# Optimization experiments

Hardware: AMD Instinct MI355X
Metric: run time of the kernel (lower is better)

Reference implementation:

```python
import jax, jax.numpy as jnp
import numpy as np

N_S = 50000   # support points
N_Q = 50000   # query points
H = 32        # neighbors per query
K = 15        # kernel points
C_IN = 64
C_OUT = 64
G = 8         # group norm groups
RADIUS = 1.0
SIGMA = 0.6
EPS = 1e-5
NEG_SLOPE = 0.1


def setup_inputs() -> dict:
    key = jax.random.key(0)
    ks = jax.random.split(key, 8)
    s_feats = jax.random.normal(ks[0], (N_S, C_IN), jnp.float32)
    q_points = jax.random.uniform(ks[1], (N_Q, 3), jnp.float32)
    s_points = jax.random.uniform(ks[2], (N_S, 3), jnp.float32)
    # index N_S is the shadow (padding) neighbor
    neighbor_indices = jax.random.randint(ks[3], (N_Q, H), 0, N_S + 1)
    # kernel point dispositions: fixed points inside a ball of RADIUS
    d = jax.random.normal(ks[4], (K, 3), jnp.float32)
    d = d / jnp.linalg.norm(d, axis=1, keepdims=True)
    r = jax.random.uniform(ks[5], (K, 1), jnp.float32) ** (1.0 / 3.0)
    kernel_points = d * r * RADIUS                      # (K,3)
    weights = jax.random.normal(ks[6], (K, C_IN, C_OUT), jnp.float32) * (1.0 / np.sqrt(K * C_IN))
    bias = jax.random.normal(ks[7], (C_OUT,), jnp.float32) * 0.01
    gamma = jnp.ones((C_OUT,), jnp.float32)
    beta = jnp.zeros((C_OUT,), jnp.float32)
    return dict(s_feats=s_feats, q_points=q_points, s_points=s_points,
                neighbor_indices=neighbor_indices, kernel_points=kernel_points,
                weights=weights, bias=bias, gamma=gamma, beta=beta)


def kpconv(s_feats, q_points, s_points, neighbor_indices, kernel_points, weights, bias):
    # pad support set with shadow point (1e10) and zero features
    pad_pts = jnp.concatenate([s_points, jnp.full((1, 3), 1e10, s_points.dtype)], axis=0)
    pad_feats = jnp.concatenate([s_feats, jnp.zeros((1, s_feats.shape[1]), s_feats.dtype)], axis=0)
    nbr_pts = pad_pts[neighbor_indices] - q_points[:, None, :]              # (M,H,3)
    diff = nbr_pts[:, :, None, :] - kernel_points[None, None, :, :]         # (M,H,K,3)
    sq_d = jnp.sum(diff * diff, axis=-1)                                    # (M,H,K)
    # linear correlation influence, clamped at 0
    w = jnp.maximum(1.0 - jnp.sqrt(sq_d) / SIGMA, 0.0)                      # (M,H,K)
    nbr_feats = pad_feats[neighbor_indices]                                 # (M,H,Cin)
    weighted = jnp.einsum('mhk,mhc->mkc', w, nbr_feats)                     # (M,K,Cin)
    out = jnp.einsum('mkc,kcd->md', weighted, weights)                      # (M,Cout)
    # normalize by number of valid neighbors (feature-sum > 0 test, as in KPConv)
    nbr_num = jnp.sum(jnp.sum(nbr_feats, axis=-1) > 0, axis=-1)             # (M,)
    nbr_num = jnp.maximum(nbr_num, 1).astype(out.dtype)
    return out / nbr_num[:, None] + bias


def group_norm(x, gamma, beta):
    # matches GroupNorm wrapper: (M,C) -> (1,C,M) -> nn.GroupNorm -> (M,C)
    M, C = x.shape
    xg = x.T.reshape(G, C // G, M)                                          # (G,Cg,M)
    mean = xg.mean(axis=(1, 2), keepdims=True)
    var = xg.var(axis=(1, 2), keepdims=True)
    xn = ((xg - mean) / jnp.sqrt(var + EPS)).reshape(C, M).T                # (M,C)
    return xn * gamma + beta


def reference(s_feats, q_points, s_points, neighbor_indices, kernel_points, weights, bias, gamma, beta):
    x = kpconv(s_feats, q_points, s_points, neighbor_indices, kernel_points, weights, bias)
    x = group_norm(x, gamma, beta)
    x = jnp.where(x >= 0, x, NEG_SLOPE * x)                                 # LeakyReLU(0.1)
    return x[:, None, :]                                                    # unsqueeze(1): (M,1,Cout)
```

## Files before the change

kernel.cpp:

```cpp
#include <hip/hip_runtime.h>
#include <hip/hip_bf16.h>
#include <math.h>

#define NSUP 50000
#define NQ   50000
#define NH   32
#define NK   15
#define NG   8
#define INV_SIGMA (1.0f/0.6f)
#define GN_EPS 1e-5f
#define NEG  0.1f

#define QB   16
#define NBLK (NQ/QB)

#define OFF_ROWSUM 0
#define OFF_FB     50048
#define OFF_WB     (OFF_FB + 1600000)
#define OFF_PS     (OFF_WB + 30720)
#define OFF_PQ     (OFF_PS + NBLK*8)
#define OFF_STAT   (OFF_PQ + NBLK*8)

typedef __attribute__((ext_vector_type(8))) short bf16x8;
typedef __attribute__((ext_vector_type(4))) float f32x4;
typedef __attribute__((ext_vector_type(4))) unsigned int u32x4;

__device__ __forceinline__ short f2bf(float x) {
    __hip_bfloat16 h = __float2bfloat16(x);
    return *reinterpret_cast<short*>(&h);
}

__global__ __launch_bounds__(256) void k_prep(const float* __restrict__ sf,
                                              float* __restrict__ rowsum,
                                              unsigned short* __restrict__ fb,
                                              const float* __restrict__ wts,
                                              unsigned short* __restrict__ wb) {
    if (blockIdx.x < 12500) {
        int row  = (blockIdx.x * 256 + threadIdx.x) >> 6;
        int lane = threadIdx.x & 63;
        if (row >= NSUP) return;
        float v = sf[(size_t)row * 64 + lane];
        fb[(size_t)row * 64 + lane] = (unsigned short)f2bf(v);
        float s = v;
        #pragma unroll
        for (int o = 32; o; o >>= 1) s += __shfl_down(s, o);
        if (lane == 0) rowsum[row] = s;
    } else {
        int idx = (blockIdx.x - 12500) * 256 + threadIdx.x;
        if (idx >= 30 * 4 * 64 * 8) return;
        int j  = idx & 7;
        int l  = (idx >> 3) & 63;
        int n  = (idx >> 9) & 3;
        int ks = idx >> 11;
        int r  = ks * 32 + ((l >> 4) << 3) + j;
        int d  = n * 16 + (l & 15);
        wb[idx] = (unsigned short)f2bf(wts[(size_t)r * 64 + d]);
    }
}

__global__ __launch_bounds__(256, 5) void k_conv(
    const unsigned short* __restrict__ fb, const float* __restrict__ qpts,
    const float* __restrict__ spts,  const int*   __restrict__ nidx,
    const float* __restrict__ kpts,  const unsigned short* __restrict__ wb,
    const float* __restrict__ bias,  const float* __restrict__ rowsum,
    float* __restrict__ conv_out, float* __restrict__ part_s, float* __restrict__ part_q)
{
    __shared__ __align__(16) short wl16[16 * 968];
    __shared__ __align__(16) float kp4[16][4];
    __shared__ float rcl[16];

    const int tid  = threadIdx.x;
    const int wv   = tid >> 6;
    const int lane = tid & 63;
    const int g    = lane >> 4;
    const int c16  = lane & 15;

    if (tid < 16) {
        if (tid < NK) {
            kp4[tid][0] = kpts[tid*3+0];
            kp4[tid][1] = kpts[tid*3+1];
            kp4[tid][2] = kpts[tid*3+2];
        } else {
            kp4[tid][0] = 1e8f; kp4[tid][1] = 1e8f; kp4[tid][2] = 1e8f;
        }
        kp4[tid][3] = 0.f;
    }
    __syncthreads();

    const float kx = kp4[c16][0], ky = kp4[c16][1], kz = kp4[c16][2];

    const int qbase = blockIdx.x * QB;
    char*  WV  = (char*)wl16 + wv * 7424;
    float* XYP = (float*)WV;
    char*  FP  = WV + 2560;

    f32x4 pacc[4][4];
    #pragma unroll
    for (int a = 0; a < 4; a++)
        #pragma unroll
        for (int b = 0; b < 4; b++) pacc[a][b] = (f32x4){0.f,0.f,0.f,0.f};

    const int h    = lane & 31;
    const int half = lane >> 5;

    #pragma unroll
    for (int pp = 0; pp < 2; pp++) {
        const int qq = pp*2 + half;
        const int m  = qbase + wv*4 + qq;
        const float qx = qpts[m*3+0], qy = qpts[m*3+1], qz = qpts[m*3+2];
        const int  id  = nidx[(size_t)m * NH + h];
        const bool val = (id < NSUP);
        const int  ii  = val ? id : 0;
        const float dx = spts[ii*3+0]-qx, dy = spts[ii*3+1]-qy, dz = spts[ii*3+2]-qz;
        const float rs = rowsum[ii];
        unsigned long long bal = __ballot(val && rs > 0.f);
        int cA = __popcll(bal & 0xffffffffull); if (cA < 1) cA = 1;
        int cB = __popcll(bal >> 32);           if (cB < 1) cB = 1;
        if (lane == 0)  rcl[wv*4 + pp*2]     = 1.0f / (float)cA;
        if (lane == 32) rcl[wv*4 + pp*2 + 1] = 1.0f / (float)cB;
        const int si = (pp*64 + half*32 + h) * 5;
        XYP[si]     = val ? dx : 1e10f;
        XYP[si + 1] = dy;
        XYP[si + 2] = dz;
    }

    const int gr = lane >> 3;
    const int gs = lane & 7;
    int   idA[4], idB[4];
    u32x4 vA[4], vB[4];
    {
        const int m0 = qbase + wv*4;
        #pragma unroll
        for (int i = 0; i < 4; i++) idA[i] = nidx[(size_t)m0*NH + i*8 + gr];
        #pragma unroll
        for (int i = 0; i < 4; i++) {
            const int id2 = (idA[i] < NSUP) ? idA[i] : 0;
            vA[i] = *(const u32x4*)((const char*)fb + (size_t)id2*128 + gs*16);
        }
        const int m1 = qbase + wv*4 + 1;
        #pragma unroll
        for (int i = 0; i < 4; i++) idB[i] = nidx[(size_t)m1*NH + i*8 + gr];
    }

    #pragma unroll
    for (int q = 0; q < 4; q++) {
        const int pp = q >> 1, e = q & 1;
        u32x4* vc  = (q & 1) ? vB  : vA;
        u32x4* vn  = (q & 1) ? vA  : vB;
        int*   idn = (q & 1) ? idA : idB;
        int*   idt = (q & 1) ? idB : idA;

        #pragma unroll
        for (int i = 0; i < 4; i++)
            *(u32x4*)(FP + (i*8 + gr)*144 + ((gs ^ i) << 4)) = vc[i];

        if (q < 3) {
            #pragma unroll
            for (int i = 0; i < 4; i++) {
                const int id2 = (idn[i] < NSUP) ? idn[i] : 0;
                vn[i] = *(const u32x4*)((const char*)fb + (size_t)id2*128 + gs*16);
            }
        }
        if (q < 2) {
            const int mn = qbase + wv*4 + q + 2;
            #pragma unroll
            for (int i = 0; i < 4; i++) idt[i] = nidx[(size_t)mn*NH + i*8 + gr];
        }

        union { unsigned short u[8]; bf16x8 v; } ua;
        #pragma unroll
        for (int j = 0; j < 8; j++) {
            const int xi = (pp*64 + e*32 + g*8 + j) * 5;
            const float px = XYP[xi], py = XYP[xi+1], pz = XYP[xi+2];
            const float ex = px - kx, ey = py - ky, ez = pz - kz;
            const float sq = fmaf(ex, ex, fmaf(ey, ey, ez * ez));
            const float w  = fmaxf(1.0f - sqrtf(sq) * INV_SIGMA, 0.f);
            ua.u[j] = (unsigned short)f2bf(w);
        }

        #pragma unroll
        for (int ct = 0; ct < 4; ct++) {
            const char* vb = FP + (g*8)*144
                           + (((((ct << 1) | (c16 >> 3)) ^ g) & 7) << 4)
                           + ((c16 & 7) << 1);
            union { unsigned short u[8]; bf16x8 v; } ub;
            #pragma unroll
            for (int j = 0; j < 8; j++)
                ub.u[j] = *(const unsigned short*)(vb + j*144);
            pacc[q][ct] = __builtin_amdgcn_mfma_f32_16x16x32_bf16(ua.v, ub.v, pacc[q][ct], 0, 0, 0);
        }
    }

    __syncthreads();

    #pragma unroll
    for (int qq = 0; qq < 4; qq++) {
        #pragma unroll
        for (int ct = 0; ct < 4; ct++) {
            #pragma unroll
            for (int i = 0; i < 4; i++) {
                const int kk = g*4 + i;
                if (kk < NK)
                    wl16[(wv*4 + qq)*968 + kk*64 + ct*16 + c16] = f2bf(pacc[qq][ct][i]);
            }
        }
    }
    __syncthreads();

    f32x4 facc = (f32x4){0.f,0.f,0.f,0.f};
    const int z = lane >> 4;
    const short* ap = wl16 + c16*968 + z*8;
    const unsigned short* bp = wb + ((size_t)(wv * 64 + lane)) * 8;
    #pragma unroll 6
    for (int ks = 0; ks < 30; ks++) {
        bf16x8 a = *(const bf16x8*)(ap + ks*32);
        bf16x8 b = *(const bf16x8*)(bp + (size_t)ks*2048);
        facc = __builtin_amdgcn_mfma_f32_16x16x32_bf16(a, b, facc, 0, 0, 0);
    }

    const int   d  = wv*16 + c16;
    const float bs = bias[d];
    float gl = 0.f, gq = 0.f;
    #pragma unroll
    for (int i = 0; i < 4; i++) {
        const int row = z*4 + i;
        const float y = facc[i] * rcl[row] + bs;
        conv_out[(size_t)(qbase + row)*64 + d] = y;
        gl += y;
        gq = fmaf(y, y, gq);
    }
    #pragma unroll
    for (int msk = 1; msk <= 4; msk <<= 1) { gl += __shfl_xor(gl, msk); gq += __shfl_xor(gq, msk); }
    gl += __shfl_xor(gl, 16); gq += __shfl_xor(gq, 16);
    gl += __shfl_xor(gl, 32); gq += __shfl_xor(gq, 32);
    if ((lane & 55) == 0) {
        const int grp = wv*2 + (lane >> 3);
        part_s[(size_t)blockIdx.x * 8 + grp] = gl;
        part_q[(size_t)blockIdx.x * 8 + grp] = gq;
    }
}

__global__ __launch_bounds__(1024) void k_reduce(const float* __restrict__ part_s,
                                                 const float* __restrict__ part_q,
                                                 float* __restrict__ stat) {
    __shared__ double ds[128][8], dq[128][8];
    const int t = threadIdx.x;
    const int g = t & 7, chunk = t >> 3;
    const int per = (NBLK + 127) / 128;
    double s = 0.0, q = 0.0;
    int lo = chunk * per, hi = lo + per; if (hi > NBLK) hi = NBLK;
    for (int i = lo; i < hi; i++) {
        s += (double)part_s[(size_t)i * 8 + g];
        q += (double)part_q[(size_t)i * 8 + g];
    }
    ds[chunk][g] = s; dq[chunk][g] = q;
    __syncthreads();
    if (t < 8) {
        double S = 0.0, Q = 0.0;
        for (int cix = 0; cix < 128; cix++) { S += ds[cix][t]; Q += dq[cix][t]; }
        const double cnt = (double)(64 / NG) * (double)NQ;
        double mean = S / cnt;
        double var  = Q / cnt - mean * mean;
        stat[t]     = (float)mean;
        stat[8 + t] = (float)(1.0 / sqrt(var + (double)GN_EPS));
    }
}

__global__ __launch_bounds__(256) void k_apply(float* __restrict__ out,
                                               const float* __restrict__ stat,
                                               const float* __restrict__ gamma,
                                               const float* __restrict__ beta) {
    const int n4 = NQ * 64 / 4;
    for (int idx = blockIdx.x * 256 + threadIdx.x; idx < n4; idx += gridDim.x * 256) {
        float4 v = ((const float4*)out)[idx];
        const int c4 = idx & 15;
        const int g  = c4 >> 1;
        const float mean = stat[g], istd = stat[8 + g];
        const float4 ga = ((const float4*)gamma)[c4];
        const float4 be = ((const float4*)beta)[c4];
        float4 r;
        r.x = (v.x - mean) * istd * ga.x + be.x; r.x = r.x >= 0.f ? r.x : NEG * r.x;
        r.y = (v.y - mean) * istd * ga.y + be.y; r.y = r.y >= 0.f ? r.y : NEG * r.y;
        r.z = (v.z - mean) * istd * ga.z + be.z; r.z = r.z >= 0.f ? r.z : NEG * r.z;
        r.w = (v.w - mean) * istd * ga.w + be.w; r.w = r.w >= 0.f ? r.w : NEG * r.w;
        ((float4*)out)[idx] = r;
    }
}

extern "C" void kernel_launch(void* const* d_in, const int* in_sizes, int n_in,
                              void* d_out, int out_size, void* d_ws, size_t ws_size,
                              hipStream_t stream) {
    const float* sfeats = (const float*)d_in[0];
    const float* qpts   = (const float*)d_in[1];
    const float* spts   = (const float*)d_in[2];
    const int*   nidx   = (const int*)  d_in[3];
    const float* kpts   = (const float*)d_in[4];
    const float* wts    = (const float*)d_in[5];
    const float* bias   = (const float*)d_in[6];
    const float* gamma  = (const float*)d_in[7];
    const float* beta   = (const float*)d_in[8];

    float* ws = (float*)d_ws;
    float*          rowsum = ws + OFF_ROWSUM;
    unsigned short* fb     = (unsigned short*)(ws + OFF_FB);
    unsigned short* wb     = (unsigned short*)(ws + OFF_WB);
    float*          ps     = ws + OFF_PS;
    float*          pq     = ws + OFF_PQ;
    float*          stat   = ws + OFF_STAT;
    float*          out    = (float*)d_out;

    k_prep <<<dim3(12740), dim3(256), 0, stream>>>(sfeats, rowsum, fb, wts, wb);
    k_conv <<<dim3(NBLK),  dim3(256), 0, stream>>>(fb, qpts, spts, nidx, kpts,
                                                   wb, bias, rowsum, out, ps, pq);
    k_reduce<<<dim3(1),    dim3(1024), 0, stream>>>(ps, pq, stat);
    k_apply <<<dim3(1024), dim3(256), 0, stream>>>(out, stat, gamma, beta);
}
```

Baseline: 77.80 us.

## Fold group-norm reduction into apply kernel and tighten LDS layouts in conv

Removes the single-block reduce kernel: each apply block now redundantly reduces the per-block partial sums itself, which drops one launch and its serialized tail. In the conv kernel, relative positions are stored as padded float4 so each is read with one vector load. B-operand feature fragments are now gathered as 32-bit LDS reads and combined with byte-permute, replacing 8 separate 16-bit loads per fragment. The cost is that all 1024 apply blocks each re-read about 25k partial values, and the conv LDS stride is shrunk to match the new layout.

Result: slower. 97.95 us (+25.9%).

```diff
diff --git a/kernel.cpp b/kernel.cpp
--- a/kernel.cpp
+++ b/kernel.cpp
@@ -19,7 +19,6 @@
 #define OFF_WB     (OFF_FB + 1600000)
 #define OFF_PS     (OFF_WB + 30720)
 #define OFF_PQ     (OFF_PS + NBLK*8)
-#define OFF_STAT   (OFF_PQ + NBLK*8)
 
 typedef __attribute__((ext_vector_type(8))) short bf16x8;
 typedef __attribute__((ext_vector_type(4))) float f32x4;
@@ -90,9 +89,9 @@
     const float kx = kp4[c16][0], ky = kp4[c16][1], kz = kp4[c16][2];
 
     const int qbase = blockIdx.x * QB;
-    char*  WV  = (char*)wl16 + wv * 7424;
-    float* XYP = (float*)WV;
-    char*  FP  = WV + 2560;
+    char*  WV   = (char*)wl16 + wv * 6656;
+    f32x4* XYP4 = (f32x4*)WV;
+    char*  FP   = WV + 2048;
 
     f32x4 pacc[4][4];
     #pragma unroll
@@ -118,10 +117,8 @@
         int cB = __popcll(bal >> 32);           if (cB < 1) cB = 1;
         if (lane == 0)  rcl[wv*4 + pp*2]     = 1.0f / (float)cA;
         if (lane == 32) rcl[wv*4 + pp*2 + 1] = 1.0f / (float)cB;
-        const int si = (pp*64 + half*32 + h) * 5;
-        XYP[si]     = val ? dx : 1e10f;
-        XYP[si + 1] = dy;
-        XYP[si + 2] = dz;
+        f32x4 st; st.x = val ? dx : 1e10f; st.y = dy; st.z = dz; st.w = 0.f;
+        XYP4[pp*64 + half*32 + h] = st;
     }
 
     const int gr = lane >> 3;
@@ -142,6 +139,8 @@
         for (int i = 0; i < 4; i++) idB[i] = nidx[(size_t)m1*NH + i*8 + gr];
     }
 
+    const unsigned selp = 0x05040100u + ((c16 & 1) ? 0x02020202u : 0u);
+
     #pragma unroll
     for (int q = 0; q < 4; q++) {
         const int pp = q >> 1, e = q & 1;
@@ -170,9 +169,8 @@
         union { unsigned short u[8]; bf16x8 v; } ua;
         #pragma unroll
         for (int j = 0; j < 8; j++) {
-            const int xi = (pp*64 + e*32 + g*8 + j) * 5;
-            const float px = XYP[xi], py = XYP[xi+1], pz = XYP[xi+2];
-            const float ex = px - kx, ey = py - ky, ez = pz - kz;
+            const f32x4 p = XYP4[pp*64 + e*32 + g*8 + j];
+            const float ex = p.x - kx, ey = p.y - ky, ez = p.z - kz;
             const float sq = fmaf(ex, ex, fmaf(ey, ey, ez * ez));
             const float w  = fmaxf(1.0f - sqrtf(sq) * INV_SIGMA, 0.f);
             ua.u[j] = (unsigned short)f2bf(w);
@@ -180,13 +178,16 @@
 
         #pragma unroll
         for (int ct = 0; ct < 4; ct++) {
-            const char* vb = FP + (g*8)*144
+            const char* vb = FP + g*1152
                            + (((((ct << 1) | (c16 >> 3)) ^ g) & 7) << 4)
-                           + ((c16 & 7) << 1);
-            union { unsigned short u[8]; bf16x8 v; } ub;
+                           + ((c16 & 6) << 1);
+            union { unsigned u32[4]; bf16x8 v; } ub;
             #pragma unroll
-            for (int j = 0; j < 8; j++)
-                ub.u[j] = *(const unsigned short*)(vb + j*144);
+            for (int t = 0; t < 4; t++) {
+                const unsigned D0 = *(const unsigned*)(vb + t*288);
+                const unsigned D1 = *(const unsigned*)(vb + t*288 + 144);
+                ub.u32[t] = __builtin_amdgcn_perm(D1, D0, selp);
+            }
             pacc[q][ct] = __builtin_amdgcn_mfma_f32_16x16x32_bf16(ua.v, ub.v, pacc[q][ct], 0, 0, 0);
         }
     }
@@ -240,42 +241,44 @@
     }
 }
 
-__global__ __launch_bounds__(1024) void k_reduce(const float* __restrict__ part_s,
-                                                 const float* __restrict__ part_q,
-                                                 float* __restrict__ stat) {
-    __shared__ double ds[128][8], dq[128][8];
-    const int t = threadIdx.x;
-    const int g = t & 7, chunk = t >> 3;
-    const int per = (NBLK + 127) / 128;
-    double s = 0.0, q = 0.0;
-    int lo = chunk * per, hi = lo + per; if (hi > NBLK) hi = NBLK;
-    for (int i = lo; i < hi; i++) {
-        s += (double)part_s[(size_t)i * 8 + g];
-        q += (double)part_q[(size_t)i * 8 + g];
-    }
-    ds[chunk][g] = s; dq[chunk][g] = q;
-    __syncthreads();
-    if (t < 8) {
-        double S = 0.0, Q = 0.0;
-        for (int cix = 0; cix < 128; cix++) { S += ds[cix][t]; Q += dq[cix][t]; }
-        const double cnt = (double)(64 / NG) * (double)NQ;
-        double mean = S / cnt;
-        double var  = Q / cnt - mean * mean;
-        stat[t]     = (float)mean;
-        stat[8 + t] = (float)(1.0 / sqrt(var + (double)GN_EPS));
-    }
-}
-
 __global__ __launch_bounds__(256) void k_apply(float* __restrict__ out,
-                                               const float* __restrict__ stat,
+                                               const float* __restrict__ part_s,
+                                               const float* __restrict__ part_q,
                                                const float* __restrict__ gamma,
                                                const float* __restrict__ beta) {
+    __shared__ double ds[32][8], dq[32][8];
+    __shared__ float st[16];
+    const int t = threadIdx.x;
+
+    {
+        const int gg = t & 7, chunk = t >> 3;
+        const int per = (NBLK + 31) / 32;
+        double s = 0.0, q = 0.0;
+        int lo = chunk * per, hi = lo + per; if (hi > NBLK) hi = NBLK;
+        for (int i = lo; i < hi; i++) {
+            s += (double)part_s[(size_t)i * 8 + gg];
+            q += (double)part_q[(size_t)i * 8 + gg];
+        }
+        ds[chunk][gg] = s; dq[chunk][gg] = q;
+        __syncthreads();
+        if (t < 8) {
+            double S = 0.0, Q = 0.0;
+            for (int cix = 0; cix < 32; cix++) { S += ds[cix][t]; Q += dq[cix][t]; }
+            const double cnt = (double)(64 / NG) * (double)NQ;
+            double mean = S / cnt;
+            double var  = Q / cnt - mean * mean;
+            st[t]     = (float)mean;
+            st[8 + t] = (float)(1.0 / sqrt(var + (double)GN_EPS));
+        }
+        __syncthreads();
+    }
+
     const int n4 = NQ * 64 / 4;
-    for (int idx = blockIdx.x * 256 + threadIdx.x; idx < n4; idx += gridDim.x * 256) {
+    for (int idx = blockIdx.x * 256 + t; idx < n4; idx += gridDim.x * 256) {
         float4 v = ((const float4*)out)[idx];
         const int c4 = idx & 15;
         const int g  = c4 >> 1;
-        const float mean = stat[g], istd = stat[8 + g];
+        const float mean = st[g], istd = st[8 + g];
         const float4 ga = ((const float4*)gamma)[c4];
         const float4 be = ((const float4*)beta)[c4];
         float4 r;
@@ -306,12 +309,10 @@
     unsigned short* wb     = (unsigned short*)(ws + OFF_WB);
     float*          ps     = ws + OFF_PS;
     float*          pq     = ws + OFF_PQ;
-    float*          stat   = ws + OFF_STAT;
     float*          out    = (float*)d_out;
 
     k_prep <<<dim3(12740), dim3(256), 0, stream>>>(sfeats, rowsum, fb, wts, wb);
     k_conv <<<dim3(NBLK),  dim3(256), 0, stream>>>(fb, qpts, spts, nidx, kpts,
                                                    wb, bias, rowsum, out, ps, pq);
-    k_reduce<<<dim3(1),    dim3(1024), 0, stream>>>(ps, pq, stat);
-    k_apply <<<dim3(1024), dim3(256), 0, stream>>>(out, stat, gamma, beta);
-}
+    k_apply<<<dim3(1024),  dim3(256), 0, stream>>>(out, ps, pq, gamma, beta);
+}
```
